# Kernel optimization log

Hardware: AMD Instinct MI355X
Metric: run time of the kernel (lower is better)

The kernel has to match this reference:

```python
import jax, jax.numpy as jnp
import numpy as np

EMBED_DIM = 128

def setup_inputs() -> dict:
    key = jax.random.key(0)
    k_x, k_wf, k_bf, k_wo, k_bo = jax.random.split(key, 5)
    C = EMBED_DIM
    x = jax.random.normal(k_x, (4, 4096, C), dtype=jnp.float32)
    # Linear(C, 3C): weight applied as x @ W_fc + b_fc with W_fc [C, 3C]
    W_fc = jax.random.normal(k_wf, (C, 3 * C), dtype=jnp.float32) * (1.0 / np.sqrt(C))
    b_fc = jax.random.normal(k_bf, (3 * C,), dtype=jnp.float32) * 0.01
    W_out = jax.random.normal(k_wo, (C, C), dtype=jnp.float32) * (1.0 / np.sqrt(C))
    b_out = jax.random.normal(k_bo, (C,), dtype=jnp.float32) * 0.01
    scale = jnp.ones((1,), dtype=jnp.float32)
    return {"x": x, "W_fc": W_fc, "b_fc": b_fc, "W_out": W_out, "b_out": b_out, "scale": scale}

def reference(x, W_fc, b_fc, W_out, b_out, scale):
    C = x.shape[-1]
    qkv = x @ W_fc + b_fc                      # [B, N, 3C]
    q, k, v = jnp.split(qkv, 3, axis=-1)       # each [B, N, C]
    # scores: [B, N, N], scaled by 1/sqrt(C) then by learnable 1/scale
    attn = jnp.einsum('bnc,bmc->bnm', q, k) / jnp.sqrt(jnp.float32(C))
    attn = jax.nn.softmax(attn / scale[0], axis=-1)
    out = jnp.einsum('bnm,bmc->bnc', attn, v)   # [B, N, C]
    return out @ W_out + b_out
```

## Files before the change

### kernel.cpp

```cpp
#include <hip/hip_runtime.h>
#include <math.h>


typedef __attribute__((ext_vector_type(8))) short bf16x8;
typedef __attribute__((ext_vector_type(4))) float f32x4;
typedef __attribute__((ext_vector_type(2))) unsigned int u32x2;

#define M2EXP 17.3124f

static __device__ __forceinline__ short f2bf(float f) {
    union { float f; unsigned int u; } c; c.f = f;
    unsigned int u = c.u;
    unsigned int r = (u + 0x7FFFu + ((u >> 16) & 1u)) >> 16;
    return (short)(r & 0xFFFFu);
}
static __device__ __forceinline__ float bf2f(short v) {
    union { unsigned int u; float f; } c;
    c.u = ((unsigned int)(unsigned short)v) << 16;
    return c.f;
}
static __device__ __forceinline__ unsigned int cvt_pk_bf16(float lo, float hi) {
    unsigned int r;
    asm("v_cvt_pk_bf16_f32 %0, %1, %2" : "=v"(r) : "v"(lo), "v"(hi));
    return r;
}

__global__ __launch_bounds__(256) void transpose_w(const float* __restrict__ Wfc,
                                                   const float* __restrict__ Wout,
                                                   short* __restrict__ WfcT,
                                                   short* __restrict__ WoT) {
    __shared__ short T[64][72];
    const int bid = blockIdx.x;
    const float* src; short* dst; int S, n0, k0;
    if (bid < 12) { src = Wfc; dst = WfcT; S = 384; n0 = (bid % 6) * 64; k0 = (bid / 6) * 64; }
    else { int b2 = bid - 12; src = Wout; dst = WoT; S = 128; n0 = (b2 & 1) * 64; k0 = (b2 >> 1) * 64; }
    const int t = threadIdx.x;
    {
        int kk = t >> 4, nn = (t & 15) * 4;
        for (int it = 0; it < 4; ++it) {
            int k = kk + it * 16;
            float4 f = *(const float4*)&src[(k0 + k) * S + n0 + nn];
            short4 s4;
            s4.x = f2bf(f.x); s4.y = f2bf(f.y); s4.z = f2bf(f.z); s4.w = f2bf(f.w);
            *(short4*)&T[k][nn] = s4;
        }
    }
    __syncthreads();
    {
        int nl = t >> 2, kg = (t & 3) * 16;
        bf16x8 v0, v1;
        for (int j = 0; j < 8; ++j) { v0[j] = T[kg + j][nl]; v1[j] = T[kg + 8 + j][nl]; }
        *(bf16x8*)&dst[(n0 + nl) * 128 + k0 + kg] = v0;
        *(bf16x8*)&dst[(n0 + nl) * 128 + k0 + kg + 8] = v1;
    }
}

__global__ __launch_bounds__(256) void qkv_kernel(
    const float* __restrict__ x, const short* __restrict__ WfcT,
    const float* __restrict__ bfc, const float* __restrict__ scale,
    short* __restrict__ Qs, short* __restrict__ Kb, short* __restrict__ VT) {
    __shared__ short Xs[32][136];
    __shared__ short Vs[128][40];
    __shared__ short QKs[32][264];
    const int t = threadIdx.x;
    const int rb = blockIdx.x;
    const int lane = t & 63, w = t >> 6;
    const int m16 = lane & 15, quad = lane >> 4;
    {
        int row = t >> 3, cg = t & 7;
        const float* src = &x[(rb * 32 + row) * 128 + cg * 16];
        float4 f0 = *(const float4*)&src[0];
        float4 f1 = *(const float4*)&src[4];
        float4 f2 = *(const float4*)&src[8];
        float4 f3 = *(const float4*)&src[12];
        bf16x8 v0, v1;
        v0[0] = f2bf(f0.x); v0[1] = f2bf(f0.y); v0[2] = f2bf(f0.z); v0[3] = f2bf(f0.w);
        v0[4] = f2bf(f1.x); v0[5] = f2bf(f1.y); v0[6] = f2bf(f1.z); v0[7] = f2bf(f1.w);
        v1[0] = f2bf(f2.x); v1[1] = f2bf(f2.y); v1[2] = f2bf(f2.z); v1[3] = f2bf(f2.w);
        v1[4] = f2bf(f3.x); v1[5] = f2bf(f3.y); v1[6] = f2bf(f3.z); v1[7] = f2bf(f3.w);
        *(bf16x8*)&Xs[row][cg * 16] = v0;
        *(bf16x8*)&Xs[row][cg * 16 + 8] = v1;
    }
    __syncthreads();

    bf16x8 a[2][4];
    for (int rt = 0; rt < 2; ++rt)
        for (int kc = 0; kc < 4; ++kc)
            a[rt][kc] = *(const bf16x8*)&Xs[rt * 16 + m16][kc * 32 + quad * 8];

    const float sfac = 1.44269504088896f / (sqrtf(128.0f) * scale[0]);

#pragma unroll
    for (int i = 0; i < 6; ++i) {
        const int gct = w * 6 + i;
        bf16x8 bfr[4];
        for (int kc = 0; kc < 4; ++kc)
            bfr[kc] = *(const bf16x8*)&WfcT[(gct * 16 + m16) * 128 + kc * 32 + quad * 8];
        f32x4 acc[2];
        for (int rt = 0; rt < 2; ++rt)
            for (int j = 0; j < 4; ++j) acc[rt][j] = 0.0f;
        for (int kc = 0; kc < 4; ++kc) {
            acc[0] = __builtin_amdgcn_mfma_f32_16x16x32_bf16(a[0][kc], bfr[kc], acc[0], 0, 0, 0);
            acc[1] = __builtin_amdgcn_mfma_f32_16x16x32_bf16(a[1][kc], bfr[kc], acc[1], 0, 0, 0);
        }
        const int c = gct * 16 + m16;
        const float bias = bfc[c];
        if (gct < 8) {
            for (int rt = 0; rt < 2; ++rt)
                for (int r = 0; r < 4; ++r)
                    QKs[rt * 16 + quad * 4 + r][c] = f2bf((acc[rt][r] + bias) * sfac);
        } else if (gct < 16) {
            for (int rt = 0; rt < 2; ++rt)
                for (int r = 0; r < 4; ++r)
                    QKs[rt * 16 + quad * 4 + r][136 + (c - 128)] = f2bf(acc[rt][r] + bias);
        } else {
            const int ch = c - 256;
            for (int rt = 0; rt < 2; ++rt)
                for (int r = 0; r < 4; ++r)
                    Vs[ch][rt * 16 + quad * 4 + r] = f2bf(acc[rt][r] + bias);
        }
    }
    __syncthreads();
    {
        int row = t >> 3, colw = (t & 7) * 16;
        short* qdst = &Qs[(rb * 32 + row) * 128 + colw];
        *(uint4*)&qdst[0] = *(const uint4*)&QKs[row][colw];
        *(uint4*)&qdst[8] = *(const uint4*)&QKs[row][colw + 8];
        short* kdst = &Kb[(rb * 32 + row) * 128 + colw];
        *(uint4*)&kdst[0] = *(const uint4*)&QKs[row][136 + colw];
        *(uint4*)&kdst[8] = *(const uint4*)&QKs[row][136 + colw + 8];
    }
    {
        int ch = t >> 1, seg = t & 1;
        int b_ = (rb * 32) >> 12, nn = (rb * 32) & 4095;
        uint4 u0 = *(const uint4*)&Vs[ch][seg * 16];
        uint4 u1 = *(const uint4*)&Vs[ch][seg * 16 + 8];
        short* dstp = &VT[((size_t)b_ * 128 + ch) * 4096 + nn + seg * 16];
        *(uint4*)&dstp[0] = u0;
        *(uint4*)&dstp[8] = u1;
    }
}

__global__ __launch_bounds__(256, 2) void flash_kernel(
    const short* __restrict__ Qs, const short* __restrict__ Kb,
    const short* __restrict__ VT, short* __restrict__ Opart,
    float* __restrict__ Lpart, int nsplit) {
    __shared__ short Kst[2 * 64 * 128];
    __shared__ short VTs[2 * 128 * 64];
    __shared__ short Ps[128 * 64];

    const int t = threadIdx.x;
    const int lane = t & 63, w = t >> 6;
    const int m16 = lane & 15, quad = lane >> 4;
    const int kvq = blockIdx.x >> 7;
    const int bqt = blockIdx.x & 127;
    const int batch = bqt & 3;
    const int qt = bqt >> 2;
    const int iters = 64 / nsplit;
    const int qlen = 4096 / nsplit;

    bf16x8 qf[2][4];
    for (int rh = 0; rh < 2; ++rh) {
        const short* qb = Qs + (batch * 4096 + qt * 128 + w * 32 + rh * 16 + m16) * 128;
        for (int kc = 0; kc < 4; ++kc)
            qf[rh][kc] = *(const bf16x8*)&qb[kc * 32 + quad * 8];
    }

    f32x4 acc_o[2][8];
    for (int rh = 0; rh < 2; ++rh)
        for (int i = 0; i < 8; ++i)
            for (int j = 0; j < 4; ++j) acc_o[rh][i][j] = 0.0f;
    float lsum[2] = {0.f, 0.f};

    const short* kbase = Kb + (batch * 4096 + kvq * qlen) * 128;
    const short* vbase = VT + (batch * 128) * 4096 + kvq * qlen;

    const int krl = lane >> 4, kslot = lane & 15;
    const int vrl = lane >> 3, vslot = lane & 7;
    const int qs7 = m16 & 7;

#define STAGE_KV(TILE, BUF)                                                       \
    {                                                                             \
        const int koff_ = (BUF) * (64 * 128);                                     \
        const int voff_ = (BUF) * (128 * 64);                                     \
        for (int j = 0; j < 4; ++j) {                                             \
            int krow = w * 16 + j * 4 + krl;                                      \
            int gch = kslot ^ (krow & 15);                                        \
            __builtin_amdgcn_global_load_lds(                                     \
                (const __attribute__((address_space(1))) void*)                   \
                    &kbase[((TILE) * 64 + krow) * 128 + gch * 8],                 \
                (__attribute__((address_space(3))) void*)                         \
                    &Kst[koff_ + (w * 16 + j * 4) * 128],                         \
                16, 0, 0);                                                        \
        }                                                                         \
        for (int j = 0; j < 4; ++j) {                                             \
            int vrow = w * 32 + j * 8 + vrl;                                      \
            int gch = vslot ^ (vrow & 7);                                         \
            __builtin_amdgcn_global_load_lds(                                     \
                (const __attribute__((address_space(1))) void*)                   \
                    &vbase[vrow * 4096 + (TILE) * 64 + gch * 8],                  \
                (__attribute__((address_space(3))) void*)                         \
                    &VTs[voff_ + (w * 32 + j * 8) * 64],                          \
                16, 0, 0);                                                        \
        }                                                                         \
    }

#define COMPUTE_TILE(BUF)                                                         \
    {                                                                             \
        const int koff_ = (BUF) * (64 * 128);                                     \
        const int voff_ = (BUF) * (128 * 64);                                     \
        f32x4 s[2][4];                                                            \
        for (int rh = 0; rh < 2; ++rh)                                            \
            for (int i = 0; i < 4; ++i)                                           \
                for (int j = 0; j < 4; ++j) s[rh][i][j] = 0.0f;                   \
        __builtin_amdgcn_s_setprio(1);                                            \
        for (int kc = 0; kc < 4; ++kc) {                                          \
            for (int ct = 0; ct < 4; ++ct) {                                      \
                bf16x8 ak = *(const bf16x8*)&Kst[koff_ + (ct * 16 + m16) * 128 +  \
                                                 (((4 * kc + quad) ^ m16) << 3)]; \
                s[0][ct] = __builtin_amdgcn_mfma_f32_16x16x32_bf16(               \
                    ak, qf[0][kc], s[0][ct], 0, 0, 0);                            \
                s[1][ct] = __builtin_amdgcn_mfma_f32_16x16x32_bf16(               \
                    ak, qf[1][kc], s[1][ct], 0, 0, 0);                            \
            }                                                                     \
        }                                                                         \
        __builtin_amdgcn_s_setprio(0);                                            \
        for (int rh = 0; rh < 2; ++rh) {                                          \
            const int q_ = w * 32 + rh * 16 + m16;                                \
            for (int ct = 0; ct < 4; ++ct) {                                      \
                float p0 = __builtin_amdgcn_exp2f(s[rh][ct][0] - M2EXP);          \
                float p1 = __builtin_amdgcn_exp2f(s[rh][ct][1] - M2EXP);          \
                float p2 = __builtin_amdgcn_exp2f(s[rh][ct][2] - M2EXP);          \
                float p3 = __builtin_amdgcn_exp2f(s[rh][ct][3] - M2EXP);          \
                lsum[rh] += (p0 + p1) + (p2 + p3);                                \
                u32x2 pw;                                                         \
                pw[0] = cvt_pk_bf16(p0, p1);                                      \
                pw[1] = cvt_pk_bf16(p2, p3);                                      \
                const int c16_ = ct * 2 + (quad >> 1);                            \
                *(u32x2*)&Ps[q_ * 64 + ((c16_ ^ qs7) << 3) + ((quad & 1) << 2)] = \
                    pw;                                                           \
            }                                                                     \
        }                                                                         \
        __builtin_amdgcn_s_setprio(1);                                            \
        for (int kc2 = 0; kc2 < 2; ++kc2) {                                       \
            bf16x8 a2[2];                                                         \
            for (int rh = 0; rh < 2; ++rh) {                                      \
                const int q_ = w * 32 + rh * 16 + m16;                            \
                a2[rh] = *(const bf16x8*)&Ps[q_ * 64 +                            \
                                             (((kc2 * 4 + quad) ^ qs7) << 3)];    \
            }                                                                     \
            for (int ot = 0; ot < 8; ++ot) {                                      \
                int vr_ = ot * 16 + m16;                                          \
                bf16x8 b2 = *(const bf16x8*)&VTs[voff_ + vr_ * 64 +               \
                                                 (((4 * kc2 + quad) ^ (vr_ & 7)) << 3)]; \
                acc_o[0][ot] = __builtin_amdgcn_mfma_f32_16x16x32_bf16(           \
                    a2[0], b2, acc_o[0][ot], 0, 0, 0);                            \
                acc_o[1][ot] = __builtin_amdgcn_mfma_f32_16x16x32_bf16(           \
                    a2[1], b2, acc_o[1][ot], 0, 0, 0);                            \
            }                                                                     \
        }                                                                         \
        __builtin_amdgcn_s_setprio(0);                                            \
    }

    STAGE_KV(0, 0);
    for (int kt = 0; kt < iters; kt += 2) {
        __syncthreads();
        STAGE_KV(kt + 1, 1);
        COMPUTE_TILE(0);
        __syncthreads();
        if (kt + 2 < iters) STAGE_KV(kt + 2, 0);
        COMPUTE_TILE(1);
    }
#undef STAGE_KV
#undef COMPUTE_TILE

    for (int rh = 0; rh < 2; ++rh) {
        lsum[rh] += __shfl_xor(lsum[rh], 16, 64);
        lsum[rh] += __shfl_xor(lsum[rh], 32, 64);
    }

    __syncthreads();
    short* Ot = Kst;
    for (int rh = 0; rh < 2; ++rh)
        for (int ot = 0; ot < 8; ++ot)
            for (int r = 0; r < 4; ++r) {
                int row = w * 32 + rh * 16 + quad * 4 + r;
                int col = ot * 16 + m16;
                Ot[row * 128 + ((((col >> 3) ^ (row & 15)) << 3)) + (col & 7)] =
                    f2bf(acc_o[rh][ot][r]);
            }
    if (quad == 0) {
        for (int rh = 0; rh < 2; ++rh) {
            const int rowb = batch * 4096 + qt * 128 + w * 32 + rh * 16 + m16;
            Lpart[kvq * 16384 + rowb] = lsum[rh];
        }
    }
    __syncthreads();
    {
        short* obase = Opart + (size_t)kvq * 16384 * 128 +
                       (size_t)(batch * 4096 + qt * 128) * 128;
        int c = t & 15;
        for (int p = 0; p < 8; ++p) {
            int row = p * 16 + (t >> 4);
            uint4 v = *(const uint4*)&Ot[row * 128 + ((c ^ (row & 15)) << 3)];
            *(uint4*)&obase[row * 128 + c * 8] = v;
        }
    }
}

__global__ __launch_bounds__(256) void mergeproj_kernel(
    const short* __restrict__ Opart, const float* __restrict__ Lpart,
    const short* __restrict__ WoT, const float* __restrict__ bout,
    float* __restrict__ out, int nsplit) {
    __shared__ short Os[16][136];
    const int t = threadIdx.x;
    const int rb = blockIdx.x;
    const int lane = t & 63, w = t >> 6;
    const int m16 = lane & 15, quad = lane >> 4;
    {
        int row = rb * 16 + (t >> 4), col = (t & 15) * 8;
        float a[8] = {0, 0, 0, 0, 0, 0, 0, 0};
        float lt = 0;
        for (int q = 0; q < nsplit; ++q) {
            bf16x8 v8 = *(const bf16x8*)&Opart[((size_t)q * 16384 + row) * 128 + col];
            for (int j = 0; j < 8; ++j) a[j] += bf2f(v8[j]);
            lt += Lpart[q * 16384 + row];
        }
        float rl = 1.0f / lt;
        bf16x8 v;
        for (int j = 0; j < 8; ++j) v[j] = f2bf(a[j] * rl);
        *(bf16x8*)&Os[t >> 4][col] = v;
    }
    __syncthreads();
    f32x4 acc[2];
    for (int i = 0; i < 2; ++i)
        for (int j = 0; j < 4; ++j) acc[i][j] = 0.0f;
    for (int kc = 0; kc < 4; ++kc) {
        bf16x8 a = *(const bf16x8*)&Os[m16][kc * 32 + quad * 8];
        for (int c2 = 0; c2 < 2; ++c2) {
            int ct = w * 2 + c2;
            bf16x8 b = *(const bf16x8*)&WoT[(ct * 16 + m16) * 128 + kc * 32 + quad * 8];
            acc[c2] = __builtin_amdgcn_mfma_f32_16x16x32_bf16(a, b, acc[c2], 0, 0, 0);
        }
    }
    for (int c2 = 0; c2 < 2; ++c2) {
        int ct = w * 2 + c2;
        int c = ct * 16 + m16;
        float bias = bout[c];
        for (int r = 0; r < 4; ++r)
            out[(rb * 16 + quad * 4 + r) * 128 + c] = acc[c2][r] + bias;
    }
}

extern "C" void kernel_launch(void* const* d_in, const int* in_sizes, int n_in,
                              void* d_out, int out_size, void* d_ws, size_t ws_size,
                              hipStream_t stream) {
    const float* x     = (const float*)d_in[0];
    const float* Wfc   = (const float*)d_in[1];
    const float* bfc   = (const float*)d_in[2];
    const float* Wout  = (const float*)d_in[3];
    const float* bout  = (const float*)d_in[4];
    const float* scale = (const float*)d_in[5];
    float* out = (float*)d_out;

    char* ws = (char*)d_ws;
    short* WfcT = (short*)(ws);
    short* WoT  = (short*)(ws + 98304);
    short* Qs   = (short*)(ws + 131072);
    short* Kb   = (short*)(ws + 131072 + 4194304);
    short* VT   = (short*)(ws + 131072 + 2 * 4194304);
    const size_t base = 131072 + (size_t)3 * 4194304;
    short* Opart = (short*)(ws + base);
    const size_t opart1 = (size_t)16384 * 128 * 2;
    const size_t lpart1 = (size_t)16384 * 4;
    int nsplit;
    if (ws_size >= base + 4 * opart1 + 4 * lpart1) nsplit = 4;
    else if (ws_size >= base + 2 * opart1 + 2 * lpart1) nsplit = 2;
    else nsplit = 1;
    float* Lpart = (float*)(ws + base + (size_t)nsplit * opart1);

    hipLaunchKernelGGL(transpose_w, dim3(16), dim3(256), 0, stream, Wfc, Wout, WfcT, WoT);
    hipLaunchKernelGGL(qkv_kernel, dim3(512), dim3(256), 0, stream, x, WfcT, bfc, scale, Qs, Kb, VT);
    hipLaunchKernelGGL(flash_kernel, dim3(128 * nsplit), dim3(256), 0, stream,
                       Qs, Kb, VT, Opart, Lpart, nsplit);
    hipLaunchKernelGGL(mergeproj_kernel, dim3(1024), dim3(256), 0, stream,
                       Opart, Lpart, WoT, bout, out, nsplit);
}
```

Measured before the change: 126.3 us.

## Split waves into 2x2 query/KV grid with in-LDS partial merge

Reassigns the four waves from 32 query rows each over all 64 KV columns to a 2x2 grid: each wave handles 64 query rows against half of the KV tile. Each K fragment loaded from LDS now feeds four MFMAs instead of two, and the V fragments are split between wave pairs. After the loop, the KV-half partial outputs and row sums are merged through shared memory before the bf16 writeback. The accumulator count doubles to 128 floats per thread, which raises register pressure and may limit occupancy at the 2-blocks launch bound. It also adds an fp32 LDS merge phase with extra barriers.

Result: slower. 214.9 us (+70.2%).

```diff
diff --git a/kernel.cpp b/kernel.cpp
--- a/kernel.cpp
+++ b/kernel.cpp
@@ -145,13 +145,16 @@
     const short* __restrict__ Qs, const short* __restrict__ Kb,
     const short* __restrict__ VT, short* __restrict__ Opart,
     float* __restrict__ Lpart, int nsplit) {
-    __shared__ short Kst[2 * 64 * 128];
-    __shared__ short VTs[2 * 128 * 64];
-    __shared__ short Ps[128 * 64];
+    __shared__ __align__(16) char smem[81920];
+    short* Kst = (short*)smem;
+    short* VTs = (short*)(smem + 32768);
+    short* Ps  = (short*)(smem + 65536);
 
     const int t = threadIdx.x;
     const int lane = t & 63, w = t >> 6;
     const int m16 = lane & 15, quad = lane >> 4;
+    const int qh = w >> 1;
+    const int kvh = w & 1;
     const int kvq = blockIdx.x >> 7;
     const int bqt = blockIdx.x & 127;
     const int batch = bqt & 3;
@@ -159,18 +162,18 @@
     const int iters = 64 / nsplit;
     const int qlen = 4096 / nsplit;
 
-    bf16x8 qf[2][4];
-    for (int rh = 0; rh < 2; ++rh) {
-        const short* qb = Qs + (batch * 4096 + qt * 128 + w * 32 + rh * 16 + m16) * 128;
+    bf16x8 qf[4][4];
+    for (int rh = 0; rh < 4; ++rh) {
+        const short* qb = Qs + (batch * 4096 + qt * 128 + qh * 64 + rh * 16 + m16) * 128;
         for (int kc = 0; kc < 4; ++kc)
             qf[rh][kc] = *(const bf16x8*)&qb[kc * 32 + quad * 8];
     }
 
-    f32x4 acc_o[2][8];
-    for (int rh = 0; rh < 2; ++rh)
+    f32x4 acc_o[4][8];
+    for (int rh = 0; rh < 4; ++rh)
         for (int i = 0; i < 8; ++i)
             for (int j = 0; j < 4; ++j) acc_o[rh][i][j] = 0.0f;
-    float lsum[2] = {0.f, 0.f};
+    float lsum[4] = {0.f, 0.f, 0.f, 0.f};
 
     const short* kbase = Kb + (batch * 4096 + kvq * qlen) * 128;
     const short* vbase = VT + (batch * 128) * 4096 + kvq * qlen;
@@ -209,25 +212,29 @@
     {                                                                             \
         const int koff_ = (BUF) * (64 * 128);                                     \
         const int voff_ = (BUF) * (128 * 64);                                     \
-        f32x4 s[2][4];                                                            \
-        for (int rh = 0; rh < 2; ++rh)                                            \
-            for (int i = 0; i < 4; ++i)                                           \
+        f32x4 s[4][2];                                                            \
+        for (int rh = 0; rh < 4; ++rh)                                            \
+            for (int i = 0; i < 2; ++i)                                           \
                 for (int j = 0; j < 4; ++j) s[rh][i][j] = 0.0f;                   \
         __builtin_amdgcn_s_setprio(1);                                            \
         for (int kc = 0; kc < 4; ++kc) {                                          \
-            for (int ct = 0; ct < 4; ++ct) {                                      \
-                bf16x8 ak = *(const bf16x8*)&Kst[koff_ + (ct * 16 + m16) * 128 +  \
-                                                 (((4 * kc + quad) ^ m16) << 3)]; \
+            for (int ct = 0; ct < 2; ++ct) {                                      \
+                bf16x8 ak = *(const bf16x8*)&Kst[koff_ +                          \
+                    (kvh * 32 + ct * 16 + m16) * 128 + (((4 * kc + quad) ^ m16) << 3)]; \
                 s[0][ct] = __builtin_amdgcn_mfma_f32_16x16x32_bf16(               \
                     ak, qf[0][kc], s[0][ct], 0, 0, 0);                            \
                 s[1][ct] = __builtin_amdgcn_mfma_f32_16x16x32_bf16(               \
                     ak, qf[1][kc], s[1][ct], 0, 0, 0);                            \
+                s[2][ct] = __builtin_amdgcn_mfma_f32_16x16x32_bf16(               \
+                    ak, qf[2][kc], s[2][ct], 0, 0, 0);                            \
+                s[3][ct] = __builtin_amdgcn_mfma_f32_16x16x32_bf16(               \
+                    ak, qf[3][kc], s[3][ct], 0, 0, 0);                            \
             }                                                                     \
         }                                                                         \
         __builtin_amdgcn_s_setprio(0);                                            \
-        for (int rh = 0; rh < 2; ++rh) {                                          \
-            const int q_ = w * 32 + rh * 16 + m16;                                \
-            for (int ct = 0; ct < 4; ++ct) {                                      \
+        for (int rh = 0; rh < 4; ++rh) {                                          \
+            const int q_ = qh * 64 + rh * 16 + m16;                               \
+            for (int ct = 0; ct < 2; ++ct) {                                      \
                 float p0 = __builtin_amdgcn_exp2f(s[rh][ct][0] - M2EXP);          \
                 float p1 = __builtin_amdgcn_exp2f(s[rh][ct][1] - M2EXP);          \
                 float p2 = __builtin_amdgcn_exp2f(s[rh][ct][2] - M2EXP);          \
@@ -236,27 +243,31 @@
                 u32x2 pw;                                                         \
                 pw[0] = cvt_pk_bf16(p0, p1);                                      \
                 pw[1] = cvt_pk_bf16(p2, p3);                                      \
-                const int c16_ = ct * 2 + (quad >> 1);                            \
+                const int c16_ = kvh * 4 + ct * 2 + (quad >> 1);                  \
                 *(u32x2*)&Ps[q_ * 64 + ((c16_ ^ qs7) << 3) + ((quad & 1) << 2)] = \
                     pw;                                                           \
             }                                                                     \
         }                                                                         \
         __builtin_amdgcn_s_setprio(1);                                            \
-        for (int kc2 = 0; kc2 < 2; ++kc2) {                                       \
-            bf16x8 a2[2];                                                         \
-            for (int rh = 0; rh < 2; ++rh) {                                      \
-                const int q_ = w * 32 + rh * 16 + m16;                            \
+        {                                                                         \
+            bf16x8 a2[4];                                                         \
+            for (int rh = 0; rh < 4; ++rh) {                                      \
+                const int q_ = qh * 64 + rh * 16 + m16;                           \
                 a2[rh] = *(const bf16x8*)&Ps[q_ * 64 +                            \
-                                             (((kc2 * 4 + quad) ^ qs7) << 3)];    \
+                                             (((kvh * 4 + quad) ^ qs7) << 3)];    \
             }                                                                     \
             for (int ot = 0; ot < 8; ++ot) {                                      \
                 int vr_ = ot * 16 + m16;                                          \
                 bf16x8 b2 = *(const bf16x8*)&VTs[voff_ + vr_ * 64 +               \
-                                                 (((4 * kc2 + quad) ^ (vr_ & 7)) << 3)]; \
+                                                 (((kvh * 4 + quad) ^ (vr_ & 7)) << 3)]; \
                 acc_o[0][ot] = __builtin_amdgcn_mfma_f32_16x16x32_bf16(           \
                     a2[0], b2, acc_o[0][ot], 0, 0, 0);                            \
                 acc_o[1][ot] = __builtin_amdgcn_mfma_f32_16x16x32_bf16(           \
                     a2[1], b2, acc_o[1][ot], 0, 0, 0);                            \
+                acc_o[2][ot] = __builtin_amdgcn_mfma_f32_16x16x32_bf16(           \
+                    a2[2], b2, acc_o[2][ot], 0, 0, 0);                            \
+                acc_o[3][ot] = __builtin_amdgcn_mfma_f32_16x16x32_bf16(           \
+                    a2[3], b2, acc_o[3][ot], 0, 0, 0);                            \
             }                                                                     \
         }                                                                         \
         __builtin_amdgcn_s_setprio(0);                                            \
@@ -274,25 +285,49 @@
 #undef STAGE_KV
 #undef COMPUTE_TILE
 
-    for (int rh = 0; rh < 2; ++rh) {
-        lsum[rh] += __shfl_xor(lsum[rh], 16, 64);
-        lsum[rh] += __shfl_xor(lsum[rh], 32, 64);
-    }
-
-    __syncthreads();
+    __syncthreads();
+    float* OmrgF = (float*)smem;
+    float* lsumL = (float*)(smem + 65536);
+    if (kvh) {
+        float* dst = OmrgF + qh * 8192;
+        for (int rh = 0; rh < 4; ++rh)
+            for (int ot = 0; ot < 8; ++ot)
+                *(f32x4*)&dst[(rh * 8 + ot) * 256 + lane * 4] = acc_o[rh][ot];
+        f32x4 lv; lv[0] = lsum[0]; lv[1] = lsum[1]; lv[2] = lsum[2]; lv[3] = lsum[3];
+        *(f32x4*)&lsumL[(qh * 64 + lane) * 4] = lv;
+    }
+    __syncthreads();
+    if (!kvh) {
+        const float* srcp = OmrgF + qh * 8192;
+        for (int rh = 0; rh < 4; ++rh)
+            for (int ot = 0; ot < 8; ++ot) {
+                f32x4 v = *(const f32x4*)&srcp[(rh * 8 + ot) * 256 + lane * 4];
+                for (int j = 0; j < 4; ++j) acc_o[rh][ot][j] += v[j];
+            }
+        f32x4 lv = *(const f32x4*)&lsumL[(qh * 64 + lane) * 4];
+        for (int rh = 0; rh < 4; ++rh) {
+            lsum[rh] += lv[rh];
+            lsum[rh] += __shfl_xor(lsum[rh], 16, 64);
+            lsum[rh] += __shfl_xor(lsum[rh], 32, 64);
+        }
+    }
+    __syncthreads();
+
     short* Ot = Kst;
-    for (int rh = 0; rh < 2; ++rh)
-        for (int ot = 0; ot < 8; ++ot)
-            for (int r = 0; r < 4; ++r) {
-                int row = w * 32 + rh * 16 + quad * 4 + r;
-                int col = ot * 16 + m16;
-                Ot[row * 128 + ((((col >> 3) ^ (row & 15)) << 3)) + (col & 7)] =
-                    f2bf(acc_o[rh][ot][r]);
+    if (!kvh) {
+        for (int rh = 0; rh < 4; ++rh)
+            for (int ot = 0; ot < 8; ++ot)
+                for (int r = 0; r < 4; ++r) {
+                    int row = qh * 64 + rh * 16 + quad * 4 + r;
+                    int col = ot * 16 + m16;
+                    Ot[row * 128 + ((((col >> 3) ^ (row & 15)) << 3)) + (col & 7)] =
+                        f2bf(acc_o[rh][ot][r]);
+                }
+        if (quad == 0) {
+            for (int rh = 0; rh < 4; ++rh) {
+                const int rowb = batch * 4096 + qt * 128 + qh * 64 + rh * 16 + m16;
+                Lpart[kvq * 16384 + rowb] = lsum[rh];
             }
-    if (quad == 0) {
-        for (int rh = 0; rh < 2; ++rh) {
-            const int rowb = batch * 4096 + qt * 128 + w * 32 + rh * 16 + m16;
-            Lpart[kvq * 16384 + rowb] = lsum[rh];
         }
     }
     __syncthreads();
```
